# Kernel optimization log

Hardware: AMD Instinct MI355X
Metric: run time of the kernel (lower is better)

Reference implementation:

```python
import jax, jax.numpy as jnp
import numpy as np

T, B, H, D = 1024, 4, 16, 64  # tgt/src len, batch, heads, head_dim
NEG = -1e9


def setup_inputs() -> dict:
    key = jax.random.key(0)
    k1, k2, k3, k4 = jax.random.split(key, 4)
    query = jax.random.normal(k1, (T, B, H, D), dtype=jnp.float32)
    in_proj_weight = jax.random.normal(k2, (H, D, 2 * D), dtype=jnp.float32) * (1.0 / np.sqrt(D))
    in_proj_bias = jnp.zeros((H, 2 * D), dtype=jnp.float32)
    pos_weight = jax.random.normal(k3, (B * H, T, T), dtype=jnp.float32)
    decay_weight = jax.random.normal(k4, (B * H, T, T), dtype=jnp.float32) * 0.1
    # causal additive mask (0 on/below diagonal, -1e9 above), as TAN feeds attn_mask
    attn_mask = jnp.triu(jnp.full((T, T), NEG, dtype=jnp.float32), k=1)
    # pad out last 64 key positions per batch element
    key_padding_mask = jnp.broadcast_to(jnp.arange(T) >= T - 64, (B, T))
    return {
        "query": query,
        "in_proj_weight": in_proj_weight,
        "in_proj_bias": in_proj_bias,
        "pos_weight": pos_weight,
        "decay_weight": decay_weight,
        "attn_mask": attn_mask,
        "key_padding_mask": key_padding_mask,
    }


def reference(query, in_proj_weight, in_proj_bias, pos_weight, decay_weight, attn_mask, key_padding_mask):
    t, b, h, d = query.shape
    scaling = (2 * d) ** -0.5  # pos_weight path uses (2*head_dim)^-0.5
    # per-head in-projection producing q,k (v = query itself)
    x = query.reshape(t * b, h, d).transpose(1, 0, 2)              # [H, T*B, D]
    proj = jnp.einsum('hnd,hde->hne', x, in_proj_weight) + in_proj_bias[:, None, :]
    proj = proj.transpose(1, 0, 2).reshape(t, b, h, 2 * d)          # [T, B, H, 2D]
    q, k = proj[..., :d], proj[..., d:]
    q = (q * scaling).reshape(t, b * h, d).transpose(1, 0, 2)       # [B*H, T, D]
    k = k.reshape(t, b * h, d).transpose(1, 0, 2)                   # [B*H, T, D]
    v = query.reshape(t, b * h, d).transpose(1, 0, 2)               # [B*H, T, D]
    scores = jnp.einsum('nqd,nkd->nqk', q, k)                       # [B*H, T, T]
    scores = scores + scaling * pos_weight + decay_weight + attn_mask[None]
    scores = scores.reshape(b, h, t, t)
    scores = jnp.where(key_padding_mask[:, None, None, :], NEG, scores)
    probs = jax.nn.softmax(scores.reshape(b * h, t, t), axis=-1)
    out = jnp.einsum('nqk,nkd->nqd', probs, v)                      # [B*H, T, D]
    return out.transpose(1, 0, 2).reshape(t, b, h, d)
```

## Files before the change

kernel.cpp:

```cpp
#include <hip/hip_runtime.h>
#include <hip/hip_bf16.h>
#include <stdint.h>

#define NEGV   -1000000000.0f
#define SCALING 0.08838834764831845f

typedef __attribute__((ext_vector_type(4))) float  f32x4;
typedef __attribute__((ext_vector_type(8))) short  bf16x8;
typedef __attribute__((ext_vector_type(4))) unsigned short u16x4;
typedef __attribute__((ext_vector_type(8))) unsigned short u16x8;

static __device__ __forceinline__ unsigned short f2bf(float x) {
    union { float f; unsigned int u; } v; v.f = x;
    unsigned int r = (v.u + 0x7FFF + ((v.u >> 16) & 1)) >> 16;
    return (unsigned short)r;
}

__global__ __launch_bounds__(256) void proj_kernel(
    const float* __restrict__ query,
    const float* __restrict__ W,
    const float* __restrict__ bias,
    unsigned short* __restrict__ Qb,
    unsigned short* __restrict__ Kb,
    unsigned short* __restrict__ Vt)
{
    __shared__ __align__(16) float Ws[64 * 128];
    __shared__ __align__(16) float xs[32][68];

    const int h   = blockIdx.y;
    const int tb0 = blockIdx.x * 32;
    const int tid = threadIdx.x;

    const float* Wg = W + (long)h * 64 * 128;
    #pragma unroll
    for (int k = 0; k < 8; ++k) {
        int idx = tid + k * 256;
        ((f32x4*)Ws)[idx] = ((const f32x4*)Wg)[idx];
    }
    {
        int r = tid >> 3, p = tid & 7;
        const float* src = query + (long)(tb0 + r) * 1024 + h * 64 + p * 8;
        f32x4 a = ((const f32x4*)src)[0];
        f32x4 b = ((const f32x4*)src)[1];
        *(f32x4*)&xs[r][p * 8]     = a;
        *(f32x4*)&xs[r][p * 8 + 4] = b;
    }
    __syncthreads();

    {
        int d = tid >> 2, b = tid & 3;
        u16x8 o;
        #pragma unroll
        for (int tp = 0; tp < 8; ++tp) o[tp] = f2bf(xs[4 * tp + b][d]);
        *(u16x8*)(Vt + ((long)(b * 16 + h) * 64 + d) * 1024 + (tb0 >> 2)) = o;
    }

    const int rg = tid >> 5;
    const int cg = tid & 31;
    float acc[4][4] = {};
    for (int dd = 0; dd < 64; dd += 4) {
        f32x4 xv0 = *(const f32x4*)&xs[rg * 4 + 0][dd];
        f32x4 xv1 = *(const f32x4*)&xs[rg * 4 + 1][dd];
        f32x4 xv2 = *(const f32x4*)&xs[rg * 4 + 2][dd];
        f32x4 xv3 = *(const f32x4*)&xs[rg * 4 + 3][dd];
        #pragma unroll
        for (int l = 0; l < 4; ++l) {
            f32x4 wv = *(const f32x4*)&Ws[(dd + l) * 128 + cg * 4];
            #pragma unroll
            for (int j = 0; j < 4; ++j) {
                acc[0][j] += xv0[l] * wv[j];
                acc[1][j] += xv1[l] * wv[j];
                acc[2][j] += xv2[l] * wv[j];
                acc[3][j] += xv3[l] * wv[j];
            }
        }
    }

    f32x4 bv = *(const f32x4*)(bias + h * 128 + cg * 4);
    const bool isQ = (cg < 16);
    const int d0 = isQ ? cg * 4 : cg * 4 - 64;
    unsigned short* dst = isQ ? Qb : Kb;
    const float scl = isQ ? SCALING : 1.0f;
    #pragma unroll
    for (int i = 0; i < 4; ++i) {
        int tb = tb0 + rg * 4 + i;
        int t = tb >> 2, b = tb & 3;
        int n = b * 16 + h;
        u16x4 o;
        o.x = f2bf((acc[i][0] + bv[0]) * scl);
        o.y = f2bf((acc[i][1] + bv[1]) * scl);
        o.z = f2bf((acc[i][2] + bv[2]) * scl);
        o.w = f2bf((acc[i][3] + bv[3]) * scl);
        *(u16x4*)(dst + ((long)n * 1024 + t) * 64 + d0) = o;
    }
}

__global__ __launch_bounds__(256, 2) void attn_kernel(
    const unsigned short* __restrict__ Qb,
    const unsigned short* __restrict__ Kb,
    const unsigned short* __restrict__ Vt,
    const float* __restrict__ pos,
    const float* __restrict__ dec,
    float* __restrict__ out)
{
    __shared__ __align__(16) unsigned short Klds[2][64][64];
    __shared__ __align__(16) unsigned short Vlds[2][64][64];
    __shared__ __align__(16) float bias_lds[4][16][68];
    __shared__ __align__(16) unsigned short P_lds[4][16][72];

    const int bx = blockIdx.x;
    const int n  = bx & 63, pi = bx >> 6;
    const int tid = threadIdx.x;
    const int w = tid >> 6, lane = tid & 63;
    const int lr = lane & 15, lg = lane >> 4;
    const int l8 = lane & 7,  lh = lane >> 3;
    const int sw = l8 ^ lh;

    const unsigned short* Kn = Kb + (long)n * 65536;
    const unsigned short* Vn = Vt + (long)n * 65536;
    const float* posn = pos + (long)n * 1048576;
    const float* decn = dec + (long)n * 1048576;

    f32x4  pp[4], dd[4];
    u16x8  kreg[2], vreg[2];

    auto issue = [&](int q0, int k0) {
        #pragma unroll
        for (int g = 0; g < 4; ++g) {
            const long ro = (long)(q0 + lg + 4 * g) * 1024 + k0 + 4 * lr;
            pp[g] = __builtin_nontemporal_load((const f32x4*)(posn + ro));
            dd[g] = __builtin_nontemporal_load((const f32x4*)(decn + ro));
        }
        #pragma unroll
        for (int j = 0; j < 2; ++j) {
            kreg[j] = *(const u16x8*)(Kn + (long)(k0 + 16 * w + 8 * j + lh) * 64 + 8 * sw);
            vreg[j] = *(const u16x8*)(Vn + (long)(16 * w + 8 * j + lh) * 1024 + k0 + 8 * sw);
        }
    };

    auto writeLDS = [&](int kb) {
        const int bsel = kb & 1;
        #pragma unroll
        for (int j = 0; j < 2; ++j) {
            *(u16x8*)(&Klds[bsel][0][0] + w * 1024 + j * 512 + 8 * lane) = kreg[j];
            *(u16x8*)(&Vlds[bsel][0][0] + w * 1024 + j * 512 + 8 * lane) = vreg[j];
        }
        #pragma unroll
        for (int g = 0; g < 4; ++g) {
            f32x4 bz;
            #pragma unroll
            for (int u = 0; u < 4; ++u) bz[u] = fmaf(SCALING, pp[g][u], dd[g][u]);
            *(f32x4*)&bias_lds[w][lg + 4 * g][4 * lr] = bz;
        }
    };

    unsigned short (*Pw)[72] = P_lds[w];

    for (int tile = 0; tile < 2; ++tile) {
        const int qb = tile ? (15 - pi) : pi;
        const int q0 = qb * 64 + w * 16;
        const int nkb = min(qb + 1, 15);

        const unsigned short* Qrow = Qb + ((long)n * 1024 + q0 + lr) * 64 + 8 * lg;
        bf16x8 qf0 = *(const bf16x8*)(Qrow);
        bf16x8 qf1 = *(const bf16x8*)(Qrow + 32);

        float m_j[4], l_j[4];
        f32x4 Oacc[4];
        #pragma unroll
        for (int dt = 0; dt < 4; ++dt) { f32x4 z = {0.f,0.f,0.f,0.f}; Oacc[dt] = z; }
        #pragma unroll
        for (int j = 0; j < 4; ++j) { m_j[j] = -3e38f; l_j[j] = 0.f; }

        issue(q0, 0);

        for (int kb = 0; kb < nkb; ++kb) {
            __syncthreads();
            writeLDS(kb);
            __syncthreads();
            if (kb + 1 < nkb) issue(q0, (kb + 1) * 64);

            const int bsel = kb & 1;
            const bool diag = (kb == qb);
            const int kt_lim = diag ? w : 3;

            f32x4 S[4];
            #pragma unroll
            for (int kt = 0; kt < 4; ++kt) {
                if (kt <= kt_lim) {
                    const unsigned short* Kr = &Klds[bsel][kt * 16 + lr][0];
                    bf16x8 kf0 = *(const bf16x8*)(Kr + 8 * (lg ^ (lr & 7)));
                    bf16x8 kf1 = *(const bf16x8*)(Kr + 8 * ((4 + lg) ^ (lr & 7)));
                    f32x4 z = {0.f,0.f,0.f,0.f};
                    f32x4 s = __builtin_amdgcn_mfma_f32_16x16x32_bf16(qf0, kf0, z, 0, 0, 0);
                    s = __builtin_amdgcn_mfma_f32_16x16x32_bf16(qf1, kf1, s, 0, 0, 0);
                    #pragma unroll
                    for (int j = 0; j < 4; ++j)
                        s[j] += bias_lds[w][4 * lg + j][kt * 16 + lr];
                    if (diag && kt == w) {
                        #pragma unroll
                        for (int j = 0; j < 4; ++j)
                            if (lr > 4 * lg + j) s[j] = NEGV;
                    }
                    S[kt] = s;
                } else {
                    f32x4 neg = {NEGV, NEGV, NEGV, NEGV};
                    S[kt] = neg;
                }
            }

            #pragma unroll
            for (int j = 0; j < 4; ++j) {
                float v = fmaxf(fmaxf(S[0][j], S[1][j]), fmaxf(S[2][j], S[3][j]));
                v = fmaxf(v, __shfl_xor(v, 1));
                v = fmaxf(v, __shfl_xor(v, 2));
                v = fmaxf(v, __shfl_xor(v, 4));
                v = fmaxf(v, __shfl_xor(v, 8));
                float mnew = fmaxf(m_j[j], v);
                float scale = __expf(m_j[j] - mnew);
                m_j[j] = mnew;
                l_j[j] *= scale;
                #pragma unroll
                for (int dt = 0; dt < 4; ++dt) Oacc[dt][j] *= scale;
                float psum = 0.f;
                #pragma unroll
                for (int kt = 0; kt < 4; ++kt) {
                    float p = __expf(S[kt][j] - mnew);
                    S[kt][j] = p;
                    psum += p;
                }
                psum += __shfl_xor(psum, 1);
                psum += __shfl_xor(psum, 2);
                psum += __shfl_xor(psum, 4);
                psum += __shfl_xor(psum, 8);
                l_j[j] += psum;
            }

            #pragma unroll
            for (int kt = 0; kt < 4; ++kt)
                #pragma unroll
                for (int j = 0; j < 4; ++j)
                    Pw[4 * lg + j][kt * 16 + lr] = f2bf(S[kt][j]);
            bf16x8 pf0 = *(const bf16x8*)&Pw[lr][8 * lg];
            bf16x8 pf1 = *(const bf16x8*)&Pw[lr][32 + 8 * lg];

            #pragma unroll
            for (int dt = 0; dt < 4; ++dt) {
                const unsigned short* Vr = &Vlds[bsel][dt * 16 + lr][0];
                bf16x8 vf0 = *(const bf16x8*)(Vr + 8 * (lg ^ (lr & 7)));
                bf16x8 vf1 = *(const bf16x8*)(Vr + 8 * ((4 + lg) ^ (lr & 7)));
                Oacc[dt] = __builtin_amdgcn_mfma_f32_16x16x32_bf16(pf0, vf0, Oacc[dt], 0, 0, 0);
                Oacc[dt] = __builtin_amdgcn_mfma_f32_16x16x32_bf16(pf1, vf1, Oacc[dt], 0, 0, 0);
            }
        }

        const int b = n >> 4, h = n & 15;
        #pragma unroll
        for (int j = 0; j < 4; ++j) {
            float inv = 1.0f / l_j[j];
            int t = q0 + 4 * lg + j;
            float* orow = out + ((long)t * 4 + b) * 1024 + h * 64 + lr;
            #pragma unroll
            for (int dt = 0; dt < 4; ++dt)
                orow[dt * 16] = Oacc[dt][j] * inv;
        }
    }
}

extern "C" void kernel_launch(void* const* d_in, const int* in_sizes, int n_in,
                              void* d_out, int out_size, void* d_ws, size_t ws_size,
                              hipStream_t stream) {
    const float* query = (const float*)d_in[0];
    const float* W     = (const float*)d_in[1];
    const float* bias  = (const float*)d_in[2];
    const float* pos   = (const float*)d_in[3];
    const float* dec   = (const float*)d_in[4];

    unsigned short* Qb = (unsigned short*)d_ws;
    unsigned short* Kb = Qb + (size_t)64 * 1024 * 64;
    unsigned short* Vt = Kb + (size_t)64 * 1024 * 64;
    float* out = (float*)d_out;

    proj_kernel<<<dim3(128, 16), 256, 0, stream>>>(query, W, bias, Qb, Kb, Vt);
    attn_kernel<<<512, 256, 0, stream>>>(Qb, Kb, Vt, pos, dec, out);
}
```

Baseline: 100.3 us.

## Prefetch two key blocks ahead in attention and flatten projection grid

The attention kernel now keeps two sets of prefetch registers (A/B) for the pos/decay bias, K and V tiles and issues global loads two key blocks ahead instead of one. This gives the streaming pos/decay loads more time to cover memory latency. The cost is roughly double the prefetch register footprint, which may reduce occupancy. Separately, the projection kernel's 2D grid becomes a 1D grid with the head index taken from the low bits, so consecutive blocks cover different heads.

```diff
diff --git a/kernel.cpp b/kernel.cpp
--- a/kernel.cpp
+++ b/kernel.cpp
@@ -27,8 +27,9 @@
     __shared__ __align__(16) float Ws[64 * 128];
     __shared__ __align__(16) float xs[32][68];
 
-    const int h   = blockIdx.y;
-    const int tb0 = blockIdx.x * 32;
+    const int bx  = blockIdx.x;
+    const int h   = bx & 15;
+    const int tb0 = (bx >> 4) * 32;
     const int tid = threadIdx.x;
 
     const float* Wg = W + (long)h * 64 * 128;
@@ -121,10 +122,11 @@
     const float* posn = pos + (long)n * 1048576;
     const float* decn = dec + (long)n * 1048576;
 
-    f32x4  pp[4], dd[4];
-    u16x8  kreg[2], vreg[2];
-
-    auto issue = [&](int q0, int k0) {
+    f32x4 ppA[4], ddA[4]; u16x8 krA[2], vrA[2];
+    f32x4 ppB[4], ddB[4]; u16x8 krB[2], vrB[2];
+
+    auto issue = [&](int q0, int k0, f32x4 (&pp)[4], f32x4 (&dd)[4],
+                     u16x8 (&kr)[2], u16x8 (&vr)[2]) {
         #pragma unroll
         for (int g = 0; g < 4; ++g) {
             const long ro = (long)(q0 + lg + 4 * g) * 1024 + k0 + 4 * lr;
@@ -133,17 +135,17 @@
         }
         #pragma unroll
         for (int j = 0; j < 2; ++j) {
-            kreg[j] = *(const u16x8*)(Kn + (long)(k0 + 16 * w + 8 * j + lh) * 64 + 8 * sw);
-            vreg[j] = *(const u16x8*)(Vn + (long)(16 * w + 8 * j + lh) * 1024 + k0 + 8 * sw);
+            kr[j] = *(const u16x8*)(Kn + (long)(k0 + 16 * w + 8 * j + lh) * 64 + 8 * sw);
+            vr[j] = *(const u16x8*)(Vn + (long)(16 * w + 8 * j + lh) * 1024 + k0 + 8 * sw);
         }
     };
 
-    auto writeLDS = [&](int kb) {
-        const int bsel = kb & 1;
+    auto writeLDS = [&](int bsel, f32x4 (&pp)[4], f32x4 (&dd)[4],
+                        u16x8 (&kr)[2], u16x8 (&vr)[2]) {
         #pragma unroll
         for (int j = 0; j < 2; ++j) {
-            *(u16x8*)(&Klds[bsel][0][0] + w * 1024 + j * 512 + 8 * lane) = kreg[j];
-            *(u16x8*)(&Vlds[bsel][0][0] + w * 1024 + j * 512 + 8 * lane) = vreg[j];
+            *(u16x8*)(&Klds[bsel][0][0] + w * 1024 + j * 512 + 8 * lane) = kr[j];
+            *(u16x8*)(&Vlds[bsel][0][0] + w * 1024 + j * 512 + 8 * lane) = vr[j];
         }
         #pragma unroll
         for (int g = 0; g < 4; ++g) {
@@ -172,13 +174,18 @@
         #pragma unroll
         for (int j = 0; j < 4; ++j) { m_j[j] = -3e38f; l_j[j] = 0.f; }
 
-        issue(q0, 0);
+        issue(q0, 0, ppA, ddA, krA, vrA);
+        if (nkb > 1) issue(q0, 64, ppB, ddB, krB, vrB);
 
         for (int kb = 0; kb < nkb; ++kb) {
             __syncthreads();
-            writeLDS(kb);
+            if ((kb & 1) == 0) writeLDS(0, ppA, ddA, krA, vrA);
+            else               writeLDS(1, ppB, ddB, krB, vrB);
             __syncthreads();
-            if (kb + 1 < nkb) issue(q0, (kb + 1) * 64);
+            if (kb + 2 < nkb) {
+                if ((kb & 1) == 0) issue(q0, (kb + 2) * 64, ppA, ddA, krA, vrA);
+                else               issue(q0, (kb + 2) * 64, ppB, ddB, krB, vrB);
+            }
 
             const int bsel = kb & 1;
             const bool diag = (kb == qb);
@@ -281,6 +288,6 @@
     unsigned short* Vt = Kb + (size_t)64 * 1024 * 64;
     float* out = (float*)d_out;
 
-    proj_kernel<<<dim3(128, 16), 256, 0, stream>>>(query, W, bias, Qb, Kb, Vt);
+    proj_kernel<<<2048, 256, 0, stream>>>(query, W, bias, Qb, Kb, Vt);
     attn_kernel<<<512, 256, 0, stream>>>(Qb, Kb, Vt, pos, dec, out);
 }
```

After: 109.8 us. 9.4% more time.
